# Performance work log

Measured on AMD Instinct MI355X. Metric: run time of the kernel, lower is better.

## Reference

```python
import jax, jax.numpy as jnp
import numpy as np

BS, IN_F, OUT_F = 64, 1024, 1024
P = 0.5          # dropout probability
Q_HALF = 2.0 / 2.0  # module stores q/2
STDV = 1.0 / float(np.sqrt(IN_F))


def setup_inputs() -> dict:
    key = jax.random.key(0)
    kx, kw, kb, kn = jax.random.split(key, 4)
    x = jax.random.normal(kx, (BS, IN_F), dtype=jnp.float32)
    weight = jax.random.uniform(kw, (IN_F, OUT_F), minval=-STDV, maxval=STDV, dtype=jnp.float32)
    bias = jax.random.uniform(kb, (OUT_F,), minval=-STDV, maxval=STDV, dtype=jnp.float32)
    # bernoulli(1-p)/(1-p) - 1, per-sample mask (use_same_mask=False)
    noise = jax.random.bernoulli(kn, 1.0 - P, (BS, IN_F, OUT_F)).astype(jnp.float32) / (1.0 - P) - 1.0
    return {"x": x, "weight": weight, "bias": bias, "noise": noise}


def reference(x, weight, bias, noise):
    # wq = |w|^(q/2) with eps; target_fraction=1.0 -> targeting_mask = 1
    wq = jnp.power(jnp.abs(weight) + 1e-15, Q_HALF)          # (in, out)
    w_noisy = weight[None, :, :] + wq[None, :, :] * noise    # (bS, in, out)
    # batched vector-matrix product: (bS,1,in) @ (bS,in,out) -> (bS,out)
    out = jnp.einsum('bi,bio->bo', x, w_noisy) + bias
    return out
```

## Files before the change

### kernel.cpp

```cpp
#include <hip/hip_runtime.h>
#include <cmath>


constexpr int BS    = 64;
constexpr int IN_F  = 1024;
constexpr int OUT_F = 1024;
constexpr int ICH   = 8;
constexpr int CHUNK = IN_F / ICH;

__global__ __launch_bounds__(256) void bridgeout_partial(
    const float* __restrict__ x, const float* __restrict__ w,
    const float* __restrict__ noise, float* __restrict__ partials) {
  const int ic = blockIdx.x;
  const int b  = blockIdx.y;
  const int t  = threadIdx.x;
  const int o  = t << 2;

  __shared__ float xs[CHUNK];
  if (t < CHUNK) xs[t] = x[b * IN_F + ic * CHUNK + t];
  __syncthreads();

  const float* wp = w + (size_t)(ic * CHUNK) * OUT_F + o;
  const float* np = noise + ((size_t)b * IN_F + (size_t)(ic * CHUNK)) * OUT_F + o;

  float ax = 0.f, ay = 0.f, az = 0.f, aw = 0.f;
#pragma unroll 4
  for (int i = 0; i < CHUNK; ++i) {
    const float xv = xs[i];
    const float4 w4 = *reinterpret_cast<const float4*>(wp);
    const float4 n4 = *reinterpret_cast<const float4*>(np);
    ax = fmaf(xv, fmaf(fabsf(w4.x) + 1e-15f, n4.x, w4.x), ax);
    ay = fmaf(xv, fmaf(fabsf(w4.y) + 1e-15f, n4.y, w4.y), ay);
    az = fmaf(xv, fmaf(fabsf(w4.z) + 1e-15f, n4.z, w4.z), az);
    aw = fmaf(xv, fmaf(fabsf(w4.w) + 1e-15f, n4.w, w4.w), aw);
    wp += OUT_F;
    np += OUT_F;
  }
  float4 acc = make_float4(ax, ay, az, aw);
  *reinterpret_cast<float4*>(partials + (size_t)(ic * BS + b) * OUT_F + o) = acc;
}

__global__ __launch_bounds__(256) void bridgeout_reduce(
    const float* __restrict__ partials, const float* __restrict__ bias,
    float* __restrict__ out) {
  const int idx = blockIdx.x * 256 + threadIdx.x;
  const int e = idx << 2;
  if (e >= BS * OUT_F) return;
  const int b = e >> 10;
  const int o = e & (OUT_F - 1);
  float4 a = *reinterpret_cast<const float4*>(bias + o);
#pragma unroll
  for (int c = 0; c < ICH; ++c) {
    const float4 p = *reinterpret_cast<const float4*>(
        partials + (size_t)(c * BS + b) * OUT_F + o);
    a.x += p.x; a.y += p.y; a.z += p.z; a.w += p.w;
  }
  *reinterpret_cast<float4*>(out + e) = a;
}

__global__ __launch_bounds__(256) void bridgeout_fused(
    const float* __restrict__ x, const float* __restrict__ w,
    const float* __restrict__ bias, const float* __restrict__ noise,
    float* __restrict__ out) {
  const int b = blockIdx.x;
  const int t = threadIdx.x;
  const int o = t << 2;

  __shared__ float xs[IN_F];
  for (int i = t; i < IN_F; i += 256) xs[i] = x[b * IN_F + i];
  __syncthreads();

  const float* wp = w + o;
  const float* np = noise + (size_t)b * IN_F * OUT_F + o;
  float ax = 0.f, ay = 0.f, az = 0.f, aw = 0.f;
#pragma unroll 4
  for (int i = 0; i < IN_F; ++i) {
    const float xv = xs[i];
    const float4 w4 = *reinterpret_cast<const float4*>(wp);
    const float4 n4 = *reinterpret_cast<const float4*>(np);
    ax = fmaf(xv, fmaf(fabsf(w4.x) + 1e-15f, n4.x, w4.x), ax);
    ay = fmaf(xv, fmaf(fabsf(w4.y) + 1e-15f, n4.y, w4.y), ay);
    az = fmaf(xv, fmaf(fabsf(w4.z) + 1e-15f, n4.z, w4.z), az);
    aw = fmaf(xv, fmaf(fabsf(w4.w) + 1e-15f, n4.w, w4.w), aw);
    wp += OUT_F;
    np += OUT_F;
  }
  const float4 bi = *reinterpret_cast<const float4*>(bias + o);
  float4 acc = make_float4(ax + bi.x, ay + bi.y, az + bi.z, aw + bi.w);
  *reinterpret_cast<float4*>(out + (size_t)b * OUT_F + o) = acc;
}

extern "C" void kernel_launch(void* const* d_in, const int* in_sizes, int n_in,
                              void* d_out, int out_size, void* d_ws, size_t ws_size,
                              hipStream_t stream) {
  const float* x     = (const float*)d_in[0];
  const float* w     = (const float*)d_in[1];
  const float* bias  = (const float*)d_in[2];
  const float* noise = (const float*)d_in[3];
  float* out = (float*)d_out;

  const size_t need = (size_t)ICH * BS * OUT_F * sizeof(float);
  if (ws_size >= need) {
    float* partials = (float*)d_ws;
    dim3 g1(ICH, BS);
    bridgeout_partial<<<g1, 256, 0, stream>>>(x, w, noise, partials);
    const int nthr = BS * OUT_F / 4;
    bridgeout_reduce<<<(nthr + 255) / 256, 256, 0, stream>>>(partials, bias, out);
  } else {
    bridgeout_fused<<<BS, 256, 0, stream>>>(x, w, bias, noise, out);
  }
}
```

Baseline: 48.15 us.

## Fuse split-K reduction into single kernel via shared-memory output-split blocks

Replaces the two-kernel partial-sum plus global reduce scheme with one kernel. Each block covers a 128-wide output slice for one batch row, and eight warp groups split the input dimension and reduce their partial sums in shared memory before adding bias. This removes the second launch and the global partials write and readback. In exchange each warp reads narrower contiguous segments of the weight and noise rows, and a block-level sync is added.

```diff
diff --git a/kernel.cpp b/kernel.cpp
--- a/kernel.cpp
+++ b/kernel.cpp
@@ -2,31 +2,40 @@
 #include <cmath>
 
 
-constexpr int BS    = 64;
-constexpr int IN_F  = 1024;
-constexpr int OUT_F = 1024;
-constexpr int ICH   = 8;
-constexpr int CHUNK = IN_F / ICH;
+constexpr int BS      = 64;
+constexpr int IN_F    = 1024;
+constexpr int OUT_F   = 1024;
+constexpr int OCH     = 8;
+constexpr int OBLK    = OUT_F / OCH;
+constexpr int IGROUPS = 8;
+constexpr int ICHUNK  = IN_F / IGROUPS;
+constexpr int OTHREADS = OBLK / 4;
 
-__global__ __launch_bounds__(256) void bridgeout_partial(
+__global__ __launch_bounds__(256) void bridgeout_fused_osplit(
     const float* __restrict__ x, const float* __restrict__ w,
-    const float* __restrict__ noise, float* __restrict__ partials) {
-  const int ic = blockIdx.x;
+    const float* __restrict__ bias, const float* __restrict__ noise,
+    float* __restrict__ out) {
+  const int oc = blockIdx.x;
   const int b  = blockIdx.y;
   const int t  = threadIdx.x;
-  const int o  = t << 2;
+  const int ig = t >> 5;
+  const int ot = t & 31;
+  const int o  = oc * OBLK + (ot << 2);
 
-  __shared__ float xs[CHUNK];
-  if (t < CHUNK) xs[t] = x[b * IN_F + ic * CHUNK + t];
+  __shared__ float  xs[IN_F];
+  __shared__ float4 red[IGROUPS][OTHREADS];
+
+  for (int i = t; i < IN_F; i += 256) xs[i] = x[b * IN_F + i];
   __syncthreads();
 
-  const float* wp = w + (size_t)(ic * CHUNK) * OUT_F + o;
-  const float* np = noise + ((size_t)b * IN_F + (size_t)(ic * CHUNK)) * OUT_F + o;
+  const int i0 = ig * ICHUNK;
+  const float* wp = w + (size_t)i0 * OUT_F + o;
+  const float* np = noise + ((size_t)b * IN_F + i0) * OUT_F + o;
 
   float ax = 0.f, ay = 0.f, az = 0.f, aw = 0.f;
 #pragma unroll 4
-  for (int i = 0; i < CHUNK; ++i) {
-    const float xv = xs[i];
+  for (int i = 0; i < ICHUNK; ++i) {
+    const float xv = xs[i0 + i];
     const float4 w4 = *reinterpret_cast<const float4*>(wp);
     const float4 n4 = *reinterpret_cast<const float4*>(np);
     ax = fmaf(xv, fmaf(fabsf(w4.x) + 1e-15f, n4.x, w4.x), ax);
@@ -36,58 +45,20 @@
     wp += OUT_F;
     np += OUT_F;
   }
-  float4 acc = make_float4(ax, ay, az, aw);
-  *reinterpret_cast<float4*>(partials + (size_t)(ic * BS + b) * OUT_F + o) = acc;
-}
-
-__global__ __launch_bounds__(256) void bridgeout_reduce(
-    const float* __restrict__ partials, const float* __restrict__ bias,
-    float* __restrict__ out) {
-  const int idx = blockIdx.x * 256 + threadIdx.x;
-  const int e = idx << 2;
-  if (e >= BS * OUT_F) return;
-  const int b = e >> 10;
-  const int o = e & (OUT_F - 1);
-  float4 a = *reinterpret_cast<const float4*>(bias + o);
-#pragma unroll
-  for (int c = 0; c < ICH; ++c) {
-    const float4 p = *reinterpret_cast<const float4*>(
-        partials + (size_t)(c * BS + b) * OUT_F + o);
-    a.x += p.x; a.y += p.y; a.z += p.z; a.w += p.w;
-  }
-  *reinterpret_cast<float4*>(out + e) = a;
-}
-
-__global__ __launch_bounds__(256) void bridgeout_fused(
-    const float* __restrict__ x, const float* __restrict__ w,
-    const float* __restrict__ bias, const float* __restrict__ noise,
-    float* __restrict__ out) {
-  const int b = blockIdx.x;
-  const int t = threadIdx.x;
-  const int o = t << 2;
-
-  __shared__ float xs[IN_F];
-  for (int i = t; i < IN_F; i += 256) xs[i] = x[b * IN_F + i];
+  red[ig][ot] = make_float4(ax, ay, az, aw);
   __syncthreads();
 
-  const float* wp = w + o;
-  const float* np = noise + (size_t)b * IN_F * OUT_F + o;
-  float ax = 0.f, ay = 0.f, az = 0.f, aw = 0.f;
-#pragma unroll 4
-  for (int i = 0; i < IN_F; ++i) {
-    const float xv = xs[i];
-    const float4 w4 = *reinterpret_cast<const float4*>(wp);
-    const float4 n4 = *reinterpret_cast<const float4*>(np);
-    ax = fmaf(xv, fmaf(fabsf(w4.x) + 1e-15f, n4.x, w4.x), ax);
-    ay = fmaf(xv, fmaf(fabsf(w4.y) + 1e-15f, n4.y, w4.y), ay);
-    az = fmaf(xv, fmaf(fabsf(w4.z) + 1e-15f, n4.z, w4.z), az);
-    aw = fmaf(xv, fmaf(fabsf(w4.w) + 1e-15f, n4.w, w4.w), aw);
-    wp += OUT_F;
-    np += OUT_F;
+  if (ig == 0) {
+    float4 a = red[0][ot];
+#pragma unroll
+    for (int g = 1; g < IGROUPS; ++g) {
+      const float4 p = red[g][ot];
+      a.x += p.x; a.y += p.y; a.z += p.z; a.w += p.w;
+    }
+    const float4 bi = *reinterpret_cast<const float4*>(bias + o);
+    a.x += bi.x; a.y += bi.y; a.z += bi.z; a.w += bi.w;
+    *reinterpret_cast<float4*>(out + (size_t)b * OUT_F + o) = a;
   }
-  const float4 bi = *reinterpret_cast<const float4*>(bias + o);
-  float4 acc = make_float4(ax + bi.x, ay + bi.y, az + bi.z, aw + bi.w);
-  *reinterpret_cast<float4*>(out + (size_t)b * OUT_F + o) = acc;
 }
 
 extern "C" void kernel_launch(void* const* d_in, const int* in_sizes, int n_in,
@@ -98,15 +69,8 @@
   const float* bias  = (const float*)d_in[2];
   const float* noise = (const float*)d_in[3];
   float* out = (float*)d_out;
+  (void)d_ws; (void)ws_size;
 
-  const size_t need = (size_t)ICH * BS * OUT_F * sizeof(float);
-  if (ws_size >= need) {
-    float* partials = (float*)d_ws;
-    dim3 g1(ICH, BS);
-    bridgeout_partial<<<g1, 256, 0, stream>>>(x, w, noise, partials);
-    const int nthr = BS * OUT_F / 4;
-    bridgeout_reduce<<<(nthr + 255) / 256, 256, 0, stream>>>(partials, bias, out);
-  } else {
-    bridgeout_fused<<<BS, 256, 0, stream>>>(x, w, bias, noise, out);
-  }
+  dim3 grid(OCH, BS);
+  bridgeout_fused_osplit<<<grid, 256, 0, stream>>>(x, w, bias, noise, out);
 }
```

Measured after the change: 83.21 us. +72.8%, slower.

## Fuse split-K reduction into partial kernel using last-block atomic flags

Applied to the files above, without the earlier changes.

Replaces the separate reduce kernel with a last-arriving-block pattern: each partial block stores its results with atomic stores, sets a per-batch bit flag, and the block that completes the mask sums all partials plus bias and writes the output. A tiny flag-init kernel is launched first. This is meant to remove the second kernel's launch and the full read-back pass, but it adds a kernel launch, scalar atomic stores and loads in place of float4 accesses, and the memory-ordering cost of the fetch_or.

```diff
diff --git a/kernel.cpp b/kernel.cpp
--- a/kernel.cpp
+++ b/kernel.cpp
@@ -8,15 +8,22 @@
 constexpr int ICH   = 8;
 constexpr int CHUNK = IN_F / ICH;
 
-__global__ __launch_bounds__(256) void bridgeout_partial(
+__global__ __launch_bounds__(64) void bridgeout_init_flags(unsigned int* __restrict__ flags) {
+  flags[threadIdx.x] = 0u;
+}
+
+__global__ __launch_bounds__(256) void bridgeout_partial_fused(
     const float* __restrict__ x, const float* __restrict__ w,
-    const float* __restrict__ noise, float* __restrict__ partials) {
+    const float* __restrict__ bias, const float* __restrict__ noise,
+    float* __restrict__ partials, unsigned int* __restrict__ flags,
+    float* __restrict__ out) {
   const int ic = blockIdx.x;
   const int b  = blockIdx.y;
   const int t  = threadIdx.x;
   const int o  = t << 2;
 
   __shared__ float xs[CHUNK];
+  __shared__ int sLast;
   if (t < CHUNK) xs[t] = x[b * IN_F + ic * CHUNK + t];
   __syncthreads();
 
@@ -36,26 +43,36 @@
     wp += OUT_F;
     np += OUT_F;
   }
-  float4 acc = make_float4(ax, ay, az, aw);
-  *reinterpret_cast<float4*>(partials + (size_t)(ic * BS + b) * OUT_F + o) = acc;
-}
 
-__global__ __launch_bounds__(256) void bridgeout_reduce(
-    const float* __restrict__ partials, const float* __restrict__ bias,
-    float* __restrict__ out) {
-  const int idx = blockIdx.x * 256 + threadIdx.x;
-  const int e = idx << 2;
-  if (e >= BS * OUT_F) return;
-  const int b = e >> 10;
-  const int o = e & (OUT_F - 1);
-  float4 a = *reinterpret_cast<const float4*>(bias + o);
+  float* p = partials + (size_t)(ic * BS + b) * OUT_F + o;
+  __hip_atomic_store(&p[0], ax, __ATOMIC_RELAXED, __HIP_MEMORY_SCOPE_AGENT);
+  __hip_atomic_store(&p[1], ay, __ATOMIC_RELAXED, __HIP_MEMORY_SCOPE_AGENT);
+  __hip_atomic_store(&p[2], az, __ATOMIC_RELAXED, __HIP_MEMORY_SCOPE_AGENT);
+  __hip_atomic_store(&p[3], aw, __ATOMIC_RELAXED, __HIP_MEMORY_SCOPE_AGENT);
+  __syncthreads();
+
+  if (t == 0) {
+    const unsigned int bit = 1u << ic;
+    const unsigned int old = __hip_atomic_fetch_or(&flags[b], bit, __ATOMIC_ACQ_REL,
+                                                   __HIP_MEMORY_SCOPE_AGENT);
+    sLast = ((old | bit) == 0xFFu) ? 1 : 0;
+  }
+  __syncthreads();
+
+  if (sLast) {
+    float4 a;
+    const float4 bi = *reinterpret_cast<const float4*>(bias + o);
+    a.x = bi.x; a.y = bi.y; a.z = bi.z; a.w = bi.w;
 #pragma unroll
-  for (int c = 0; c < ICH; ++c) {
-    const float4 p = *reinterpret_cast<const float4*>(
-        partials + (size_t)(c * BS + b) * OUT_F + o);
-    a.x += p.x; a.y += p.y; a.z += p.z; a.w += p.w;
+    for (int c = 0; c < ICH; ++c) {
+      const float* q = partials + (size_t)(c * BS + b) * OUT_F + o;
+      a.x += __hip_atomic_load(&q[0], __ATOMIC_RELAXED, __HIP_MEMORY_SCOPE_AGENT);
+      a.y += __hip_atomic_load(&q[1], __ATOMIC_RELAXED, __HIP_MEMORY_SCOPE_AGENT);
+      a.z += __hip_atomic_load(&q[2], __ATOMIC_RELAXED, __HIP_MEMORY_SCOPE_AGENT);
+      a.w += __hip_atomic_load(&q[3], __ATOMIC_RELAXED, __HIP_MEMORY_SCOPE_AGENT);
+    }
+    *reinterpret_cast<float4*>(out + (size_t)b * OUT_F + o) = a;
   }
-  *reinterpret_cast<float4*>(out + e) = a;
 }
 
 __global__ __launch_bounds__(256) void bridgeout_fused(
@@ -99,13 +116,15 @@
   const float* noise = (const float*)d_in[3];
   float* out = (float*)d_out;
 
-  const size_t need = (size_t)ICH * BS * OUT_F * sizeof(float);
+  const size_t partial_bytes = (size_t)ICH * BS * OUT_F * sizeof(float);
+  const size_t need = partial_bytes + BS * sizeof(unsigned int);
   if (ws_size >= need) {
     float* partials = (float*)d_ws;
+    unsigned int* flags = (unsigned int*)((char*)d_ws + partial_bytes);
+    bridgeout_init_flags<<<1, 64, 0, stream>>>(flags);
     dim3 g1(ICH, BS);
-    bridgeout_partial<<<g1, 256, 0, stream>>>(x, w, noise, partials);
-    const int nthr = BS * OUT_F / 4;
-    bridgeout_reduce<<<(nthr + 255) / 256, 256, 0, stream>>>(partials, bias, out);
+    bridgeout_partial_fused<<<g1, 256, 0, stream>>>(x, w, bias, noise,
+                                                    partials, flags, out);
   } else {
     bridgeout_fused<<<BS, 256, 0, stream>>>(x, w, bias, noise, out);
   }
```

New measurement: 74.89 us. +55.5%, slower.

## Fuse partial and reduce kernels via grid-wide atomic barrier

Applied to the files above, without the earlier changes.

Merges the partial-sum kernel and the reduction kernel into one launch. Blocks signal completion on an atomic counter, spin until all 512 have arrived, then each block reduces its slice of outputs. A tiny init kernel resets the counter. This removes one kernel launch and its gap, but it relies on all 512 blocks being co-resident, which 256 CUs at two blocks per CU should allow, and it adds spin-wait overhead.

```diff
diff --git a/kernel.cpp b/kernel.cpp
--- a/kernel.cpp
+++ b/kernel.cpp
@@ -7,10 +7,18 @@
 constexpr int OUT_F = 1024;
 constexpr int ICH   = 8;
 constexpr int CHUNK = IN_F / ICH;
+constexpr int OBLK  = OUT_F / ICH;
+constexpr unsigned NBLK = ICH * BS;
 
-__global__ __launch_bounds__(256) void bridgeout_partial(
+__global__ __launch_bounds__(64) void bridgeout_init(unsigned* __restrict__ counter) {
+  if (threadIdx.x == 0) *counter = 0u;
+}
+
+__global__ __launch_bounds__(256, 2) void bridgeout_persistent(
     const float* __restrict__ x, const float* __restrict__ w,
-    const float* __restrict__ noise, float* __restrict__ partials) {
+    const float* __restrict__ bias, const float* __restrict__ noise,
+    float* __restrict__ partials, unsigned* __restrict__ counter,
+    float* __restrict__ out) {
   const int ic = blockIdx.x;
   const int b  = blockIdx.y;
   const int t  = threadIdx.x;
@@ -36,26 +44,32 @@
     wp += OUT_F;
     np += OUT_F;
   }
-  float4 acc = make_float4(ax, ay, az, aw);
-  *reinterpret_cast<float4*>(partials + (size_t)(ic * BS + b) * OUT_F + o) = acc;
-}
+  *reinterpret_cast<float4*>(partials + (size_t)(ic * BS + b) * OUT_F + o) =
+      make_float4(ax, ay, az, aw);
 
-__global__ __launch_bounds__(256) void bridgeout_reduce(
-    const float* __restrict__ partials, const float* __restrict__ bias,
-    float* __restrict__ out) {
-  const int idx = blockIdx.x * 256 + threadIdx.x;
-  const int e = idx << 2;
-  if (e >= BS * OUT_F) return;
-  const int b = e >> 10;
-  const int o = e & (OUT_F - 1);
-  float4 a = *reinterpret_cast<const float4*>(bias + o);
+  __syncthreads();
+  if (t == 0) {
+    __hip_atomic_fetch_add(counter, 1u, __ATOMIC_RELEASE, __HIP_MEMORY_SCOPE_AGENT);
+    unsigned v = __hip_atomic_load(counter, __ATOMIC_RELAXED, __HIP_MEMORY_SCOPE_AGENT);
+    while (v < NBLK) {
+      __builtin_amdgcn_s_sleep(2);
+      v = __hip_atomic_load(counter, __ATOMIC_RELAXED, __HIP_MEMORY_SCOPE_AGENT);
+    }
+    (void)__hip_atomic_load(counter, __ATOMIC_ACQUIRE, __HIP_MEMORY_SCOPE_AGENT);
+  }
+  __syncthreads();
+
+  if (t < OBLK / 4) {
+    const int oo = ic * OBLK + (t << 2);
+    float4 a = *reinterpret_cast<const float4*>(bias + oo);
 #pragma unroll
-  for (int c = 0; c < ICH; ++c) {
-    const float4 p = *reinterpret_cast<const float4*>(
-        partials + (size_t)(c * BS + b) * OUT_F + o);
-    a.x += p.x; a.y += p.y; a.z += p.z; a.w += p.w;
+    for (int c = 0; c < ICH; ++c) {
+      const float4 p = *reinterpret_cast<const float4*>(
+          partials + (size_t)(c * BS + b) * OUT_F + oo);
+      a.x += p.x; a.y += p.y; a.z += p.z; a.w += p.w;
+    }
+    *reinterpret_cast<float4*>(out + (size_t)b * OUT_F + oo) = a;
   }
-  *reinterpret_cast<float4*>(out + e) = a;
 }
 
 __global__ __launch_bounds__(256) void bridgeout_fused(
@@ -99,13 +113,15 @@
   const float* noise = (const float*)d_in[3];
   float* out = (float*)d_out;
 
-  const size_t need = (size_t)ICH * BS * OUT_F * sizeof(float);
+  const size_t partial_bytes = (size_t)ICH * BS * OUT_F * sizeof(float);
+  const size_t need = partial_bytes + sizeof(unsigned);
   if (ws_size >= need) {
     float* partials = (float*)d_ws;
+    unsigned* counter = (unsigned*)((char*)d_ws + partial_bytes);
+    bridgeout_init<<<1, 64, 0, stream>>>(counter);
     dim3 g1(ICH, BS);
-    bridgeout_partial<<<g1, 256, 0, stream>>>(x, w, noise, partials);
-    const int nthr = BS * OUT_F / 4;
-    bridgeout_reduce<<<(nthr + 255) / 256, 256, 0, stream>>>(partials, bias, out);
+    bridgeout_persistent<<<g1, 256, 0, stream>>>(x, w, bias, noise,
+                                                 partials, counter, out);
   } else {
     bridgeout_fused<<<BS, 256, 0, stream>>>(x, w, bias, noise, out);
   }
```

Result: slower. 102.6 us (+113.0%).
